# Performance work log

Hardware: AMD Instinct MI355X
Metric: run time of the kernel (lower is better)

Reference implementation:

```python
import jax, jax.numpy as jnp
import numpy as np

DIM = 768
NUM_HEADS = 12
HEAD_DIM = DIM // NUM_HEADS
WS = 14                       # window_size (14, 14)
N_TOK = WS * WS + 1           # 197 (patches + cls)
NUM_REL = (2 * WS - 1) ** 2 + 3  # 732
SCALE = HEAD_DIM ** -0.5


def _build_rel_index():
    # Faithful port of the BEiT relative_position_index construction.
    coords = np.stack(np.meshgrid(np.arange(WS), np.arange(WS), indexing='ij'))  # (2, WS, WS)
    flat = coords.reshape(2, -1)                                   # (2, WS*WS)
    rel = flat[:, :, None] - flat[:, None, :]                      # (2, P, P)
    rel = rel.transpose(1, 2, 0).astype(np.int64)                  # (P, P, 2)
    rel[:, :, 0] += WS - 1
    rel[:, :, 1] += WS - 1
    rel[:, :, 0] *= 2 * WS - 1
    idx = np.zeros((N_TOK, N_TOK), dtype=np.int64)
    idx[1:, 1:] = rel.sum(-1)
    idx[0, :] = NUM_REL - 3
    idx[:, 0] = NUM_REL - 2
    idx[0, 0] = NUM_REL - 1
    return idx


def setup_inputs() -> dict:
    key = jax.random.key(0)
    ks = jax.random.split(key, 7)
    B = 64
    x = jax.random.normal(ks[0], (B, N_TOK, DIM), dtype=jnp.float32)
    qkv_w = jax.random.normal(ks[1], (3 * DIM, DIM), dtype=jnp.float32) * 0.02
    q_bias = jnp.zeros((DIM,), dtype=jnp.float32)
    v_bias = jnp.zeros((DIM,), dtype=jnp.float32)
    rel_table = jax.random.normal(ks[2], (NUM_REL, NUM_HEADS), dtype=jnp.float32) * 0.02
    proj_w = jax.random.normal(ks[3], (DIM, DIM), dtype=jnp.float32) * 0.02
    proj_b = jnp.zeros((DIM,), dtype=jnp.float32)
    rel_index = jnp.asarray(_build_rel_index())  # (N, N) int64
    return {"x": x, "qkv_w": qkv_w, "q_bias": q_bias, "v_bias": v_bias,
            "rel_table": rel_table, "proj_w": proj_w, "proj_b": proj_b,
            "rel_index": rel_index}


def reference(x, qkv_w, q_bias, v_bias, rel_table, proj_w, proj_b, rel_index):
    B, N, C = x.shape
    # qkv bias = concat(q_bias, zeros, v_bias)
    qkv_b = jnp.concatenate([q_bias, jnp.zeros_like(v_bias), v_bias])
    qkv = x @ qkv_w.T + qkv_b                       # (B, N, 3C)
    qkv = qkv.reshape(B, N, 3, NUM_HEADS, HEAD_DIM).transpose(2, 0, 3, 1, 4)
    q, k, v = qkv[0], qkv[1], qkv[2]                # each (B, H, N, hd)
    attn = jnp.einsum('bhqd,bhkd->bhqk', q * SCALE, k)
    # relative position bias gathered from table: (N, N, H) -> (H, N, N)
    bias = rel_table[rel_index].transpose(2, 0, 1)
    attn = attn + bias[None]
    attn = jax.nn.softmax(attn, axis=-1)
    out = jnp.einsum('bhqk,bhkd->bhqd', attn, v)    # (B, H, N, hd)
    out = out.transpose(0, 2, 1, 3).reshape(B, N, -1)
    return out @ proj_w.T + proj_b
```

## Files before the change

### kernel.cpp

```cpp
#include <hip/hip_runtime.h>
#include <stdint.h>

#define NTOK 197
#define HD 64
#define NH 12
#define CDIM 768
#define BB 64
#define MTOT (BB*NTOK)
#define MPAD 12672
#define SCALE 0.125f
#define BTP 208

typedef __attribute__((ext_vector_type(8))) short short8;
typedef __attribute__((ext_vector_type(4))) float f32x4;
typedef unsigned short us;

__device__ __forceinline__ us f2b(float f){
    union { float f; uint32_t u; } v; v.f = f;
    uint32_t u = v.u;
    uint32_t r = u + 0x7fffu + ((u >> 16) & 1u);
    return (us)(r >> 16);
}

__device__ __forceinline__ float b2f(us b){
    union { uint32_t u; float f; } v; v.u = ((uint32_t)b) << 16;
    return v.f;
}

__device__ __forceinline__ void gload16(const us* g, us* l){
    __builtin_amdgcn_global_load_lds((const __attribute__((address_space(1))) void*)g,
                                     (__attribute__((address_space(3))) void*)l, 16, 0, 0);
}

#define LGKM0_BAR() do{ asm volatile("s_waitcnt lgkmcnt(0)" ::: "memory"); \
                        __builtin_amdgcn_s_barrier(); }while(0)

__device__ __forceinline__ void cvt4(const float* in, us* out, int i){
    float4 v = ((const float4*)in)[i];
    ushort4 o;
    o.x = f2b(v.x); o.y = f2b(v.y); o.z = f2b(v.z); o.w = f2b(v.w);
    ((ushort4*)out)[i] = o;
}

__global__ void prep_kernel(const float* __restrict__ x, const float* __restrict__ qkv_w,
                            const float* __restrict__ proj_w,
                            const int* __restrict__ rel_index, const float* __restrict__ rel_table,
                            us* __restrict__ xb, us* __restrict__ wqkv, us* __restrict__ wproj,
                            float* __restrict__ biasT)
{
    const int N1 = MTOT*CDIM/4;
    const int N2 = 3*CDIM*CDIM/4;
    const int N3 = CDIM*CDIM/4;
    const int N4 = BTP*BTP;
    const int total = N1+N2+N3+N4;
    for (int i = blockIdx.x*blockDim.x + threadIdx.x; i < total; i += gridDim.x*blockDim.x){
        if (i < N1) cvt4(x, xb, i);
        else if (i < N1+N2) cvt4(qkv_w, wqkv, i-N1);
        else if (i < N1+N2+N3) cvt4(proj_w, wproj, i-N1-N2);
        else {
            int t = i - N1 - N2 - N3;
            int col = t / BTP, row = t - col*BTP;
            if (row < NTOK && col < NTOK){
                int idx = rel_index[row*NTOK + col];
                #pragma unroll
                for (int h = 0; h < NH; ++h)
                    biasT[((size_t)h*BTP + col)*BTP + row] = rel_table[idx*NH + h];
            } else {
                #pragma unroll
                for (int h = 0; h < NH; ++h)
                    biasT[((size_t)h*BTP + col)*BTP + row] = 0.f;
            }
        }
    }
}

__global__ __launch_bounds__(512,2) void pgemm6_kernel(
    const us* __restrict__ A, const us* __restrict__ Bw,
    us* __restrict__ Qo, us* __restrict__ Ko, us* __restrict__ Vo,
    const float* __restrict__ b0, const float* __restrict__ b2, int ny, int total)
{
    __shared__ __align__(16) us AsB[3][12288];
    us* cbuf = &AsB[2][0];
    const int tid  = threadIdx.x;
    const int lane = tid & 63;
    const int wave = tid >> 6;
    const int wrr = wave >> 2;
    const int wcc = wave & 3;
    const int lr = lane & 15;
    const int g  = lane >> 4;

    const int id  = blockIdx.x;
    const int xcd = id & 7;
    const int jb  = id >> 3;
    const int qs  = total >> 3, rs = total & 7;
    const int Ssp = xcd*qs + (xcd < rs ? xcd : rs);
    const int L   = qs + (xcd < rs ? 1 : 0);
    const int qb  = L >> 6, rb = L & 63;
    const int cnt = qb + (jb < rb ? 1 : 0);
    const int w0  = Ssp + jb*qb + (jb < rb ? jb : rb);
    if (cnt == 0) return;

    int aoff, aldo, bofs[2], bldo[2];
    {
        int c = tid;
        int row = c >> 2, ch = c & 3;
        aoff = row*CDIM + ((ch ^ ((row >> 1) & 3))*8);
        aldo = c*8;
    }
    #pragma unroll
    for (int jj=0;jj<2;jj++){
        int c = tid + jj*512;
        int row = c >> 2, ch = c & 3;
        bofs[jj] = row*CDIM + ((ch ^ ((row >> 1) & 3))*8);
        bldo[jj] = 4096 + c*8;
    }

    const int S = cnt * 24;
    auto stageStep = [&](int x){
        int tt = x / 24, kt = x - tt*24;
        int ww = w0 + tt;
        int bx = ww / ny, by = ww - bx*ny;
        const us* pA = A  + (size_t)(bx*128)*CDIM;
        const us* pB = Bw + (size_t)(by*256)*CDIM;
        int buf = x % 3;
        gload16(pA + aoff + kt*32, &AsB[buf][aldo]);
        #pragma unroll
        for (int jj=0;jj<2;jj++) gload16(pB + bofs[jj] + kt*32, &AsB[buf][bldo[jj]]);
    };

    stageStep(0);
    if (S > 1) stageStep(1);
    int s = 0;

    const int co = 8*(g ^ ((lr >> 1) & 3));

    #pragma unroll 1
    for (int tt = 0; tt < cnt; ++tt){
        const int w  = w0 + tt;
        const int bx = w / ny, by = w - bx*ny;
        const int m0 = bx*128, n0 = by*256;
        const int whc = n0 / CDIM;
        float addf[4];
        const float sclf = (whc == 0) ? SCALE : 1.f;
        #pragma unroll
        for (int nt=0;nt<4;nt++){
            int n = n0 + wcc*64 + nt*16 + lr;
            int hn = n - whc*CDIM;
            addf[nt] = (whc == 0) ? b0[hn] : (whc == 2 ? b2[hn] : 0.f);
        }

        f32x4 acc[4][4];
        #pragma unroll
        for (int i=0;i<4;i++)
            #pragma unroll
            for (int jj=0;jj<4;jj++) acc[i][jj] = (f32x4){0.f,0.f,0.f,0.f};

        #pragma unroll 1
        for (int kt = 0; kt < 24; ++kt){
            if (s == S-1) asm volatile("s_waitcnt vmcnt(0)" ::: "memory");
            else          asm volatile("s_waitcnt vmcnt(3)" ::: "memory");
            __builtin_amdgcn_s_barrier();
            if (s + 2 < S) stageStep(s + 2);
            const us* la = &AsB[s % 3][0];
            const us* lb = &AsB[s % 3][4096];
            short8 af[4], bf[4];
            #pragma unroll
            for (int mt=0;mt<4;mt++)
                af[mt] = *(const short8*)&la[(wrr*64+mt*16+lr)*32 + co];
            #pragma unroll
            for (int nt=0;nt<4;nt++)
                bf[nt] = *(const short8*)&lb[(wcc*64+nt*16+lr)*32 + co];
            __builtin_amdgcn_s_setprio(1);
            #pragma unroll
            for (int mt=0;mt<4;mt++)
                #pragma unroll
                for (int nt=0;nt<4;nt++)
                    acc[mt][nt] = __builtin_amdgcn_mfma_f32_16x16x32_bf16(af[mt], bf[nt], acc[mt][nt], 0,0,0);
            __builtin_amdgcn_s_setprio(0);
            ++s;
        }

        LGKM0_BAR();

        const us* outp = (whc == 0 ? Qo : (whc == 1 ? Ko : Vo));
        #pragma unroll 1
        for (int ph = 0; ph < 4; ++ph){
            const int half  = ph & 1;
            const int rhalf = ph >> 1;
            if (wrr == rhalf && (wcc >> 1) == half){
                #pragma unroll
                for (int mt=0;mt<4;mt++)
                    #pragma unroll
                    for (int rr=0;rr<4;rr++){
                        int row = mt*16 + g*4 + rr;
                        #pragma unroll
                        for (int nt=0;nt<4;nt++){
                            int col = (wcc & 1)*64 + nt*16 + lr;
                            cbuf[row*132 + col] = f2b((acc[mt][nt][rr] + addf[nt]) * sclf);
                        }
                    }
            }
            LGKM0_BAR();
            #pragma unroll
            for (int p=0;p<2;p++){
                int c = tid + p*512;
                int row = c >> 4, ch = c & 15;
                int m = m0 + rhalf*64 + row;
                if (m < MTOT){
                    short8 vv = *(const short8*)&cbuf[row*132 + ch*8];
                    int n = n0 + half*128 + ch*8;
                    int hn = n - whc*CDIM;
                    int h  = hn >> 6, d0 = hn & 63;
                    int bidx = m / NTOK;
                    int tok  = m - bidx*NTOK;
                    size_t off = ((size_t)((bidx*NH + h)*NTOK + tok))*HD + d0;
                    *(short8*)((us*)outp + off) = vv;
                }
            }
            LGKM0_BAR();
        }
    }
}

__global__ __launch_bounds__(256) void proj_gemm_kernel(
    const us* __restrict__ A, const us* __restrict__ Bw,
    float* __restrict__ Cout, const float* __restrict__ b0, int ny)
{
    __shared__ __align__(16) us lds[32768];
    us* As = lds;
    us* Bs = lds + 16384;
    const int tid  = threadIdx.x;
    const int lane = tid & 63;
    const int wave = tid >> 6;
    const int wr = wave >> 1, wc = wave & 1;
    const int lr = lane & 15;
    const int g  = lane >> 4;

    const int NB   = gridDim.x;
    const int base = NB >> 3;
    const int rem  = NB & 7;
    const int id   = blockIdx.x;
    const int xcd  = id & 7;
    const int qq   = id >> 3;
    const int start = (xcd < rem) ? xcd*(base+1) : rem*(base+1) + (xcd-rem)*base;
    const int w    = start + qq;
    const int bx   = w / ny;
    const int by   = w - bx*ny;
    const int m0 = bx * 128;
    const int n0 = by * 128;
    const int NT = CDIM / 128;

    const int row0 = tid >> 4;
    const int cg   = (tid & 15) ^ row0;

    float addf[4];
    #pragma unroll
    for (int nt=0;nt<4;nt++) addf[nt] = b0[n0 + wc*64 + nt*16 + lr];

    f32x4 acc[4][4];
    #pragma unroll
    for (int i=0;i<4;i++)
        #pragma unroll
        for (int j=0;j<4;j++) acc[i][j] = (f32x4){0.f,0.f,0.f,0.f};

    const us* gA = A  + (size_t)(m0 + row0)*CDIM + cg*8;
    const us* gB = Bw + (size_t)(n0 + row0)*CDIM + cg*8;

    #pragma unroll 1
    for (int kt = 0; kt < NT; ++kt){
        __syncthreads();
        #pragma unroll
        for (int j=0;j<8;j++){
            gload16(gA + (size_t)j*16*CDIM + kt*128, As + tid*8 + j*2048);
            gload16(gB + (size_t)j*16*CDIM + kt*128, Bs + tid*8 + j*2048);
        }
        __syncthreads();
        #pragma unroll
        for (int kk=0; kk<4; ++kk){
            const int co = 8*((kk*4 + g) ^ lr);
            short8 af[4], bf[4];
            #pragma unroll
            for (int mt=0;mt<4;mt++)
                af[mt] = *(const short8*)&As[(wr*64+mt*16+lr)*128 + co];
            #pragma unroll
            for (int nt=0;nt<4;nt++)
                bf[nt] = *(const short8*)&Bs[(wc*64+nt*16+lr)*128 + co];
            __builtin_amdgcn_s_setprio(1);
            #pragma unroll
            for (int mt=0;mt<4;mt++)
                #pragma unroll
                for (int nt=0;nt<4;nt++)
                    acc[mt][nt] = __builtin_amdgcn_mfma_f32_16x16x32_bf16(af[mt], bf[nt], acc[mt][nt], 0,0,0);
            __builtin_amdgcn_s_setprio(0);
        }
    }

    __syncthreads();
    #pragma unroll
    for (int mt=0;mt<4;mt++)
        #pragma unroll
        for (int r=0;r<4;r++){
            int row = wr*64 + mt*16 + g*4 + r;
            #pragma unroll
            for (int nt=0;nt<4;nt++){
                int col = wc*64 + nt*16 + lr;
                lds[row*132 + col] = f2b(acc[mt][nt][r] + addf[nt]);
            }
        }
    __syncthreads();
    #pragma unroll
    for (int j=0;j<8;j++){
        int c2  = tid + j*256;
        int row = c2 >> 4;
        int ch  = c2 & 15;
        int m = m0 + row;
        if (m >= MTOT) continue;
        short8 vv = *(const short8*)&lds[row*132 + ch*8];
        int n = n0 + ch*8;
        float4 f0, f1;
        f0.x = b2f((us)vv[0]); f0.y = b2f((us)vv[1]); f0.z = b2f((us)vv[2]); f0.w = b2f((us)vv[3]);
        f1.x = b2f((us)vv[4]); f1.y = b2f((us)vv[5]); f1.z = b2f((us)vv[6]); f1.w = b2f((us)vv[7]);
        *(float4*)&Cout[(size_t)m*CDIM + n]     = f0;
        *(float4*)&Cout[(size_t)m*CDIM + n + 4] = f1;
    }
}

__global__ __launch_bounds__(256) void attn_kernel(
    const us* __restrict__ Q,
    const us* __restrict__ K,
    const us* __restrict__ V,
    const float* __restrict__ biasT,
    us* __restrict__ Ao)
{
    __shared__ us Vt[64][232];
    __shared__ us Ps[4][16][232];
    const int bh = blockIdx.x;
    const int b = bh / NH;
    const int h = bh - b*NH;
    const us* Qh = Q + (size_t)bh*NTOK*HD;
    const us* Kh = K + (size_t)bh*NTOK*HD;
    const us* Vh = V + (size_t)bh*NTOK*HD;
    const float* bT = biasT + (size_t)h*BTP*BTP;
    const int tid = threadIdx.x, lane = tid & 63, wave = tid >> 6;
    const int lr = lane & 15, g = lane >> 4, ko = g*8;

    for (int i = tid; i < 64*232/2; i += 256) ((uint32_t*)Vt)[i] = 0;
    __syncthreads();
    {
        int d0 = (tid & 7) * 8;
        for (int t = tid >> 3; t < NTOK; t += 32){
            short8 v = *(const short8*)&Vh[t*HD + d0];
            #pragma unroll
            for (int j=0;j<8;j++) Vt[d0+j][t] = (us)v[j];
        }
    }
    __syncthreads();

    for (int s = wave; s < 13; s += 4){
        int qrow = s*16 + lr; qrow = qrow > 196 ? 196 : qrow;
        short8 qa0 = *(const short8*)&Qh[qrow*HD + ko];
        short8 qa1 = *(const short8*)&Qh[qrow*HD + 32 + ko];
        f32x4 S[13];
        #pragma unroll
        for (int t=0;t<13;t++){
            int kc = t*16 + lr; kc = kc > 196 ? 196 : kc;
            short8 kb0 = *(const short8*)&Kh[kc*HD + ko];
            short8 kb1 = *(const short8*)&Kh[kc*HD + 32 + ko];
            f32x4 a = (f32x4){0.f,0.f,0.f,0.f};
            a = __builtin_amdgcn_mfma_f32_16x16x32_bf16(qa0, kb0, a, 0,0,0);
            a = __builtin_amdgcn_mfma_f32_16x16x32_bf16(qa1, kb1, a, 0,0,0);
            S[t] = a;
        }
        float rmax[4] = {-3e38f,-3e38f,-3e38f,-3e38f};
        #pragma unroll
        for (int t=0;t<13;t++){
            int col = t*16 + lr;
            bool cok = col < NTOK;
            float4 b4 = *(const float4*)&bT[(size_t)col*BTP + s*16 + g*4];
            #pragma unroll
            for (int r=0;r<4;r++){
                float xv = S[t][r] + ((const float*)&b4)[r];
                xv = cok ? xv : -1e30f;
                S[t][r] = xv;
                rmax[r] = fmaxf(rmax[r], xv);
            }
        }
        #pragma unroll
        for (int r=0;r<4;r++)
            #pragma unroll
            for (int msk=1; msk<16; msk<<=1)
                rmax[r] = fmaxf(rmax[r], __shfl_xor(rmax[r], msk));
        float rsum[4] = {0.f,0.f,0.f,0.f};
        #pragma unroll
        for (int t=0;t<13;t++)
            #pragma unroll
            for (int r=0;r<4;r++){
                float e = __expf(S[t][r] - rmax[r]);
                S[t][r] = e;
                rsum[r] += e;
            }
        #pragma unroll
        for (int r=0;r<4;r++){
            #pragma unroll
            for (int msk=1; msk<16; msk<<=1)
                rsum[r] += __shfl_xor(rsum[r], msk);
            rsum[r] = 1.f / rsum[r];
        }
        #pragma unroll
        for (int t=0;t<13;t++)
            #pragma unroll
            for (int r=0;r<4;r++)
                Ps[wave][g*4+r][t*16+lr] = f2b(S[t][r] * rsum[r]);
        #pragma unroll
        for (int r=0;r<4;r++) Ps[wave][g*4+r][208+lr] = 0;
        asm volatile("s_waitcnt lgkmcnt(0)" ::: "memory");
        f32x4 pv[4];
        #pragma unroll
        for (int nt=0;nt<4;nt++) pv[nt] = (f32x4){0.f,0.f,0.f,0.f};
        #pragma unroll
        for (int ks=0; ks<7; ks++){
            int k0 = ks*32 + ko;
            short8 pa = *(const short8*)&Ps[wave][lr][k0];
            #pragma unroll
            for (int nt=0;nt<4;nt++){
                short8 vb = *(const short8*)&Vt[nt*16+lr][k0];
                pv[nt] = __builtin_amdgcn_mfma_f32_16x16x32_bf16(pa, vb, pv[nt], 0,0,0);
            }
        }
        #pragma unroll
        for (int nt=0;nt<4;nt++)
            #pragma unroll
            for (int r=0;r<4;r++){
                int tok = s*16 + g*4 + r;
                if (tok < NTOK)
                    Ao[(size_t)(b*NTOK + tok)*CDIM + h*HD + nt*16 + lr] = f2b(pv[nt][r]);
            }
    }
}

extern "C" void kernel_launch(void* const* d_in, const int* in_sizes, int n_in,
                              void* d_out, int out_size, void* d_ws, size_t ws_size,
                              hipStream_t stream)
{
    const float* x        = (const float*)d_in[0];
    const float* qkv_w    = (const float*)d_in[1];
    const float* q_bias   = (const float*)d_in[2];
    const float* v_bias   = (const float*)d_in[3];
    const float* rel_tab  = (const float*)d_in[4];
    const float* proj_w   = (const float*)d_in[5];
    const float* proj_b   = (const float*)d_in[6];
    const int*   rel_idx  = (const int*)d_in[7];
    float* out = (float*)d_out;

    char* w = (char*)d_ws;
    us* xb    = (us*)w; w += (size_t)MPAD*CDIM*2;
    us* wqkv  = (us*)w; w += (size_t)3*CDIM*CDIM*2;
    us* wproj = (us*)w; w += (size_t)CDIM*CDIM*2;
    us* Qb    = (us*)w; w += (size_t)BB*NH*NTOK*HD*2;
    us* Kb    = (us*)w; w += (size_t)BB*NH*NTOK*HD*2;
    us* Vb    = (us*)w; w += (size_t)BB*NH*NTOK*HD*2;
    float* biasT = (float*)w; w += (size_t)NH*BTP*BTP*4;
    us* aob   = (us*)w; w += (size_t)MPAD*CDIM*2;

    prep_kernel<<<2048, 256, 0, stream>>>(x, qkv_w, proj_w, rel_idx, rel_tab,
                                          xb, wqkv, wproj, biasT);

    pgemm6_kernel<<<512, 512, 0, stream>>>(xb, wqkv, Qb, Kb, Vb, q_bias, v_bias, 9, 891);
    attn_kernel<<<BB*NH, 256, 0, stream>>>(Qb, Kb, Vb, biasT, aob);
    proj_gemm_kernel<<<594, 256, 0, stream>>>(aob, wproj, out, proj_b, 6);
}
```

Measured before the change: 153.4 us.

## Reuse pipelined persistent QKV GEMM kernel for output projection via epilogue template

Templates the triple-buffered, persistent 128x256-tile QKV GEMM on its epilogue and uses it for the output projection too, replacing the simpler single-buffered 128x128 proj kernel. The aim is to give the projection the same async-load pipelining and XCD-aware scheduling. In exchange the projection runs only 297 tiles spread over 512 blocks, so many blocks sit idle and per-block work is uneven, and larger tiles reduce parallelism.

```diff
diff --git a/kernel.cpp b/kernel.cpp
--- a/kernel.cpp
+++ b/kernel.cpp
@@ -74,8 +74,10 @@
     }
 }
 
+template<int EPI>
 __global__ __launch_bounds__(512,2) void pgemm6_kernel(
     const us* __restrict__ A, const us* __restrict__ Bw,
+    float* __restrict__ Cout,
     us* __restrict__ Qo, us* __restrict__ Ko, us* __restrict__ Vo,
     const float* __restrict__ b0, const float* __restrict__ b2, int ny, int total)
 {
@@ -139,14 +141,17 @@
         const int w  = w0 + tt;
         const int bx = w / ny, by = w - bx*ny;
         const int m0 = bx*128, n0 = by*256;
-        const int whc = n0 / CDIM;
+        const int whc = (EPI == 0) ? (n0 / CDIM) : 0;
         float addf[4];
-        const float sclf = (whc == 0) ? SCALE : 1.f;
+        const float sclf = (EPI == 0 && whc == 0) ? SCALE : 1.f;
         #pragma unroll
         for (int nt=0;nt<4;nt++){
             int n = n0 + wcc*64 + nt*16 + lr;
-            int hn = n - whc*CDIM;
-            addf[nt] = (whc == 0) ? b0[hn] : (whc == 2 ? b2[hn] : 0.f);
+            if (EPI == 1) addf[nt] = b0[n];
+            else {
+                int hn = n - whc*CDIM;
+                addf[nt] = (whc == 0) ? b0[hn] : (whc == 2 ? b2[hn] : 0.f);
+            }
         }
 
         f32x4 acc[4][4];
@@ -182,7 +187,7 @@
 
         LGKM0_BAR();
 
-        const us* outp = (whc == 0 ? Qo : (whc == 1 ? Ko : Vo));
+        const us* outp = (EPI == 0) ? (whc == 0 ? Qo : (whc == 1 ? Ko : Vo)) : nullptr;
         #pragma unroll 1
         for (int ph = 0; ph < 4; ++ph){
             const int half  = ph & 1;
@@ -209,119 +214,24 @@
                 if (m < MTOT){
                     short8 vv = *(const short8*)&cbuf[row*132 + ch*8];
                     int n = n0 + half*128 + ch*8;
-                    int hn = n - whc*CDIM;
-                    int h  = hn >> 6, d0 = hn & 63;
-                    int bidx = m / NTOK;
-                    int tok  = m - bidx*NTOK;
-                    size_t off = ((size_t)((bidx*NH + h)*NTOK + tok))*HD + d0;
-                    *(short8*)((us*)outp + off) = vv;
+                    if (EPI == 1){
+                        float4 f0, f1;
+                        f0.x = b2f((us)vv[0]); f0.y = b2f((us)vv[1]); f0.z = b2f((us)vv[2]); f0.w = b2f((us)vv[3]);
+                        f1.x = b2f((us)vv[4]); f1.y = b2f((us)vv[5]); f1.z = b2f((us)vv[6]); f1.w = b2f((us)vv[7]);
+                        *(float4*)&Cout[(size_t)m*CDIM + n]     = f0;
+                        *(float4*)&Cout[(size_t)m*CDIM + n + 4] = f1;
+                    } else {
+                        int hn = n - whc*CDIM;
+                        int h  = hn >> 6, d0 = hn & 63;
+                        int bidx = m / NTOK;
+                        int tok  = m - bidx*NTOK;
+                        size_t off = ((size_t)((bidx*NH + h)*NTOK + tok))*HD + d0;
+                        *(short8*)((us*)outp + off) = vv;
+                    }
                 }
             }
             LGKM0_BAR();
         }
-    }
-}
-
-__global__ __launch_bounds__(256) void proj_gemm_kernel(
-    const us* __restrict__ A, const us* __restrict__ Bw,
-    float* __restrict__ Cout, const float* __restrict__ b0, int ny)
-{
-    __shared__ __align__(16) us lds[32768];
-    us* As = lds;
-    us* Bs = lds + 16384;
-    const int tid  = threadIdx.x;
-    const int lane = tid & 63;
-    const int wave = tid >> 6;
-    const int wr = wave >> 1, wc = wave & 1;
-    const int lr = lane & 15;
-    const int g  = lane >> 4;
-
-    const int NB   = gridDim.x;
-    const int base = NB >> 3;
-    const int rem  = NB & 7;
-    const int id   = blockIdx.x;
-    const int xcd  = id & 7;
-    const int qq   = id >> 3;
-    const int start = (xcd < rem) ? xcd*(base+1) : rem*(base+1) + (xcd-rem)*base;
-    const int w    = start + qq;
-    const int bx   = w / ny;
-    const int by   = w - bx*ny;
-    const int m0 = bx * 128;
-    const int n0 = by * 128;
-    const int NT = CDIM / 128;
-
-    const int row0 = tid >> 4;
-    const int cg   = (tid & 15) ^ row0;
-
-    float addf[4];
-    #pragma unroll
-    for (int nt=0;nt<4;nt++) addf[nt] = b0[n0 + wc*64 + nt*16 + lr];
-
-    f32x4 acc[4][4];
-    #pragma unroll
-    for (int i=0;i<4;i++)
-        #pragma unroll
-        for (int j=0;j<4;j++) acc[i][j] = (f32x4){0.f,0.f,0.f,0.f};
-
-    const us* gA = A  + (size_t)(m0 + row0)*CDIM + cg*8;
-    const us* gB = Bw + (size_t)(n0 + row0)*CDIM + cg*8;
-
-    #pragma unroll 1
-    for (int kt = 0; kt < NT; ++kt){
-        __syncthreads();
-        #pragma unroll
-        for (int j=0;j<8;j++){
-            gload16(gA + (size_t)j*16*CDIM + kt*128, As + tid*8 + j*2048);
-            gload16(gB + (size_t)j*16*CDIM + kt*128, Bs + tid*8 + j*2048);
-        }
-        __syncthreads();
-        #pragma unroll
-        for (int kk=0; kk<4; ++kk){
-            const int co = 8*((kk*4 + g) ^ lr);
-            short8 af[4], bf[4];
-            #pragma unroll
-            for (int mt=0;mt<4;mt++)
-                af[mt] = *(const short8*)&As[(wr*64+mt*16+lr)*128 + co];
-            #pragma unroll
-            for (int nt=0;nt<4;nt++)
-                bf[nt] = *(const short8*)&Bs[(wc*64+nt*16+lr)*128 + co];
-            __builtin_amdgcn_s_setprio(1);
-            #pragma unroll
-            for (int mt=0;mt<4;mt++)
-                #pragma unroll
-                for (int nt=0;nt<4;nt++)
-                    acc[mt][nt] = __builtin_amdgcn_mfma_f32_16x16x32_bf16(af[mt], bf[nt], acc[mt][nt], 0,0,0);
-            __builtin_amdgcn_s_setprio(0);
-        }
-    }
-
-    __syncthreads();
-    #pragma unroll
-    for (int mt=0;mt<4;mt++)
-        #pragma unroll
-        for (int r=0;r<4;r++){
-            int row = wr*64 + mt*16 + g*4 + r;
-            #pragma unroll
-            for (int nt=0;nt<4;nt++){
-                int col = wc*64 + nt*16 + lr;
-                lds[row*132 + col] = f2b(acc[mt][nt][r] + addf[nt]);
-            }
-        }
-    __syncthreads();
-    #pragma unroll
-    for (int j=0;j<8;j++){
-        int c2  = tid + j*256;
-        int row = c2 >> 4;
-        int ch  = c2 & 15;
-        int m = m0 + row;
-        if (m >= MTOT) continue;
-        short8 vv = *(const short8*)&lds[row*132 + ch*8];
-        int n = n0 + ch*8;
-        float4 f0, f1;
-        f0.x = b2f((us)vv[0]); f0.y = b2f((us)vv[1]); f0.z = b2f((us)vv[2]); f0.w = b2f((us)vv[3]);
-        f1.x = b2f((us)vv[4]); f1.y = b2f((us)vv[5]); f1.z = b2f((us)vv[6]); f1.w = b2f((us)vv[7]);
-        *(float4*)&Cout[(size_t)m*CDIM + n]     = f0;
-        *(float4*)&Cout[(size_t)m*CDIM + n + 4] = f1;
     }
 }
 
@@ -465,7 +375,7 @@
     prep_kernel<<<2048, 256, 0, stream>>>(x, qkv_w, proj_w, rel_idx, rel_tab,
                                           xb, wqkv, wproj, biasT);
 
-    pgemm6_kernel<<<512, 512, 0, stream>>>(xb, wqkv, Qb, Kb, Vb, q_bias, v_bias, 9, 891);
+    pgemm6_kernel<0><<<512, 512, 0, stream>>>(xb, wqkv, nullptr, Qb, Kb, Vb, q_bias, v_bias, 9, 891);
     attn_kernel<<<BB*NH, 256, 0, stream>>>(Qb, Kb, Vb, biasT, aob);
-    proj_gemm_kernel<<<594, 256, 0, stream>>>(aob, wproj, out, proj_b, 6);
-}
+    pgemm6_kernel<1><<<512, 512, 0, stream>>>(aob, wproj, out, nullptr, nullptr, nullptr, proj_b, nullptr, 3, 297);
+}
```

Measured after the change: 154.8 us. Within noise of the previous version (+0.9%).
